# Optimization experiments

Hardware: AMD Instinct MI355X
Metric: run time of the kernel (lower is better)

Reference implementation:

```python
import jax, jax.numpy as jnp
import numpy as np


def setup_inputs() -> dict:
    key = jax.random.key(0)
    k1, k2, k3, k4 = jax.random.split(key, 4)
    B, S, D = 32, 512, 768
    return {
        "image": jax.random.normal(k1, (B, S, D), dtype=jnp.float32),
        "text": jax.random.normal(k2, (B, S, D), dtype=jnp.float32),
        "target": jax.random.normal(k3, (B, S, D), dtype=jnp.float32),
        "padding_mask": jax.random.randint(k4, (B, S), 0, 2, dtype=jnp.int32),
    }


def reference(image, text, target, padding_mask):
    D = image.shape[-1]
    # Drop BOS / CLS position for the text<->target alignment.
    txt = text[:, 1:]                      # [B, S-1, D]
    tgt = target[:, 1:]                    # [B, S-1, D]
    pm = padding_mask[:, 1:]               # [B, S-1]

    # Cosine similarity: normalize then batched matmul.
    txt_n = txt / jnp.linalg.norm(txt, axis=-1, keepdims=True)
    tgt_n = tgt / jnp.linalg.norm(tgt, axis=-1, keepdims=True)
    sim = jnp.einsum('bid,bjd->bij', txt_n, tgt_n)   # [B, S-1, S-1]

    # For each text token, pick the best-matching target patch.
    idx = jnp.argmax(sim, axis=-1)                   # [B, S-1]
    aligned = jnp.take_along_axis(tgt, idx[..., None], axis=1)  # [B, S-1, D]

    # Masked MSE over non-padded tokens (mask==1 means padded in torch code).
    valid = (pm == 0).astype(jnp.float32)            # [B, S-1]
    diff2 = jnp.square(txt.astype(jnp.float32) - aligned.astype(jnp.float32))
    kd_text_loss = jnp.sum(diff2 * valid[..., None]) / (jnp.sum(valid) * D)

    # Plain MSE between image tokens and full target.
    kd_image_loss = jnp.mean(jnp.square(image.astype(jnp.float32) - target.astype(jnp.float32)))

    total_loss = (kd_text_loss + kd_image_loss) / 2
    return total_loss, kd_text_loss, kd_image_loss, idx
```

## Files before the change

kernel.cpp:

```cpp
#include <hip/hip_runtime.h>
#include <math.h>

#define B       32
#define S_FULL  512
#define S       511
#define D       768
#define NROWS   (B * S)

#define TM 128
#define TN 128
#define NCHUNK 4
#define NKT 24
#define EPS_MARGIN 6e-5f
#define SIM_SCALE  512.0f

typedef __attribute__((ext_vector_type(8))) _Float16 f16x8;
typedef __attribute__((ext_vector_type(4))) float f32x4;

__device__ inline void cvt8(const float4& v0, const float4& v1, float s,
                            f16x8& hv, f16x8& lv, float& nacc) {
    float x[8] = {v0.x, v0.y, v0.z, v0.w, v1.x, v1.y, v1.z, v1.w};
    #pragma unroll
    for (int e = 0; e < 8; e += 2) {
        float xa = x[e] * s, xb = x[e + 1] * s;
        nacc = fmaf(xa, xa, nacc);
        nacc = fmaf(xb, xb, nacc);
        auto h = __builtin_amdgcn_cvt_pkrtz(xa, xb);
        auto l = __builtin_amdgcn_cvt_pkrtz(xa - (float)h.x, xb - (float)h.y);
        hv[e] = (_Float16)h.x; hv[e + 1] = (_Float16)h.y;
        lv[e] = (_Float16)l.x; lv[e + 1] = (_Float16)l.y;
    }
}

__global__ __launch_bounds__(256) void prep_kernel(
    const float* __restrict__ image, const float* __restrict__ target,
    float* __restrict__ acc)
{
    int row  = blockIdx.x * 4 + (threadIdx.x >> 6);
    int lane = threadIdx.x & 63;
    const float4* pi4 = (const float4*)(image  + (size_t)row * D);
    const float4* pg4 = (const float4*)(target + (size_t)row * D);
    float si = 0.f;
    #pragma unroll
    for (int q = 0; q < 3; ++q) {
        float4 m = pi4[lane + 64 * q];
        float4 g = pg4[lane + 64 * q];
        float dx = m.x-g.x, dy = m.y-g.y, dz = m.z-g.z, dw = m.w-g.w;
        si += dx*dx + dy*dy + dz*dz + dw*dw;
    }
    #pragma unroll
    for (int m = 32; m > 0; m >>= 1) si += __shfl_xor(si, m);
    if (lane == 0) atomicAdd(&acc[blockIdx.x & 63], si);
}

__global__ __launch_bounds__(256, 2) void simargmax_kernel(
    const float* __restrict__ text, const float* __restrict__ target,
    float* __restrict__ inv_g,
    float* __restrict__ pv, float* __restrict__ ps, int* __restrict__ pj)
{
    __shared__ __align__(16) _Float16 As[2][TM * 64];
    __shared__ __align__(16) _Float16 Bs[2][TM * 64];
    __shared__ float itL[TM], igL[TM];

    const int i0 = blockIdx.x * TM;
    const int jc = blockIdx.y;
    const int j0 = jc * TN;
    const int b  = blockIdx.z;
    const int t  = threadIdx.x;
    const int lane = t & 63;
    const int wy = t >> 6;
    const int quad = lane >> 4, cid = lane & 15;

    const float* Abase = text   + (size_t)b * S_FULL * D + D;
    const float* Bbase = target + (size_t)b * S_FULL * D + D;

    const int r0 = t >> 2;
    const int c0 = t & 3;
    const int kq = c0 * 8;

    const int sw8 = (r0 & 7) * 8;
    const int fw8 = (cid & 7) * 8;
    const int qh  = quad * 8;

    float na[2] = {0.f, 0.f}, nb[2] = {0.f, 0.f};

    f32x4 acc[2][8];
    #pragma unroll
    for (int mt = 0; mt < 2; ++mt)
        #pragma unroll
        for (int nt = 0; nt < 8; ++nt)
            acc[mt][nt] = (f32x4){0.f, 0.f, 0.f, 0.f};

    float4 va[2][2], vb[2][2];
    auto loadk = [&](int kt) {
        const int k0 = kt * 32;
        #pragma unroll
        for (int h = 0; h < 2; ++h) {
            int gi = i0 + r0 + 64 * h;
            if (gi < S) {
                const float4* pa = (const float4*)(Abase + (size_t)gi * D + k0 + kq);
                va[h][0] = pa[0]; va[h][1] = pa[1];
            } else {
                va[h][0] = make_float4(0.f,0.f,0.f,0.f);
                va[h][1] = make_float4(0.f,0.f,0.f,0.f);
            }
            int gj = j0 + r0 + 64 * h;
            if (gj < S) {
                const float4* pb = (const float4*)(Bbase + (size_t)gj * D + k0 + kq);
                vb[h][0] = pb[0]; vb[h][1] = pb[1];
            } else {
                vb[h][0] = make_float4(0.f,0.f,0.f,0.f);
                vb[h][1] = make_float4(0.f,0.f,0.f,0.f);
            }
        }
    };
    auto cvtstore = [&](int p) {
        #pragma unroll
        for (int h = 0; h < 2; ++h) {
            int base = (r0 + 64 * h) * 64;
            f16x8 hv, lv;
            cvt8(va[h][0], va[h][1], SIM_SCALE, hv, lv, na[h]);
            *(f16x8*)&As[p][base + ((c0 * 8)      ^ sw8)] = hv;
            *(f16x8*)&As[p][base + ((32 + c0 * 8) ^ sw8)] = lv;
            cvt8(vb[h][0], vb[h][1], SIM_SCALE, hv, lv, nb[h]);
            *(f16x8*)&Bs[p][base + ((c0 * 8)      ^ sw8)] = hv;
            *(f16x8*)&Bs[p][base + ((32 + c0 * 8) ^ sw8)] = lv;
        }
    };

    loadk(0);
    cvtstore(0);

    for (int kt = 0; kt < NKT; ++kt) {
        const int p = kt & 1;
        if (kt + 1 < NKT) loadk(kt + 1);
        __syncthreads();
        f16x8 ah[2], al[2];
        #pragma unroll
        for (int mt = 0; mt < 2; ++mt) {
            int ad = (wy * 32 + mt * 16 + cid) * 64;
            ah[mt] = *(const f16x8*)&As[p][ad + ( qh       ^ fw8)];
            al[mt] = *(const f16x8*)&As[p][ad + ((32 + qh) ^ fw8)];
        }
        #pragma unroll
        for (int nt = 0; nt < 8; ++nt) {
            int bd = (nt * 16 + cid) * 64;
            f16x8 bh = *(const f16x8*)&Bs[p][bd + ( qh       ^ fw8)];
            f16x8 bl = *(const f16x8*)&Bs[p][bd + ((32 + qh) ^ fw8)];
            #pragma unroll
            for (int mt = 0; mt < 2; ++mt) {
                acc[mt][nt] = __builtin_amdgcn_mfma_f32_16x16x32_f16(ah[mt], bh, acc[mt][nt], 0, 0, 0);
                acc[mt][nt] = __builtin_amdgcn_mfma_f32_16x16x32_f16(ah[mt], bl, acc[mt][nt], 0, 0, 0);
                acc[mt][nt] = __builtin_amdgcn_mfma_f32_16x16x32_f16(al[mt], bh, acc[mt][nt], 0, 0, 0);
            }
        }
        if (kt + 1 < NKT) cvtstore(p ^ 1);
    }

    float* fsA = (float*)&As[0][0];
    float* fsB = fsA + 4 * TM;
    #pragma unroll
    for (int h = 0; h < 2; ++h) {
        fsA[(r0 + 64 * h) * 4 + c0] = na[h];
        fsB[(r0 + 64 * h) * 4 + c0] = nb[h];
    }
    __syncthreads();
    if (t < TM) {
        float s = fsA[t*4] + fsA[t*4+1] + fsA[t*4+2] + fsA[t*4+3];
        itL[t] = (s > 0.f) ? (1.f / sqrtf(s)) : 0.f;
    } else {
        int r = t - TM;
        float s = fsB[r*4] + fsB[r*4+1] + fsB[r*4+2] + fsB[r*4+3];
        float ig = (s > 0.f) ? (1.f / sqrtf(s)) : 0.f;
        igL[r] = ig;
        if (i0 == 0) {
            int gj = j0 + r;
            if (gj < S) inv_g[b * S + gj] = ig;
        }
    }
    __syncthreads();

    float igr[8];
    #pragma unroll
    for (int nt = 0; nt < 8; ++nt) igr[nt] = igL[nt * 16 + cid];
    #pragma unroll
    for (int mt = 0; mt < 2; ++mt) {
        #pragma unroll
        for (int r = 0; r < 4; ++r) {
            float v1 = -INFINITY, v2 = -INFINITY; int j1 = -1;
            #pragma unroll
            for (int nt = 0; nt < 8; ++nt) {
                int col = j0 + nt * 16 + cid;
                float v = acc[mt][nt][r] * igr[nt];
                if (col < S) {
                    if (v > v1) { v2 = v1; v1 = v; j1 = col; }
                    else if (v > v2) v2 = v;
                }
            }
            #pragma unroll
            for (int m = 1; m < 16; m <<= 1) {
                float ov1 = __shfl_xor(v1, m);
                int   oj1 = __shfl_xor(j1, m);
                float ov2 = __shfl_xor(v2, m);
                if (ov1 > v1) { v2 = fmaxf(v1, ov2); v1 = ov1; j1 = oj1; }
                else          { v2 = fmaxf(v2, ov1); }
            }
            if (cid == 0) {
                int lrow = wy * 32 + mt * 16 + quad * 4 + r;
                int gi = i0 + lrow;
                if (gi < S) {
                    float it = itL[lrow];
                    size_t o = ((size_t)(b * S + gi) << 2) + jc;
                    pv[o] = v1 * it; ps[o] = v2 * it; pj[o] = j1;
                }
            }
        }
    }
}

__global__ __launch_bounds__(256) void text_kernel(
    const float* __restrict__ text, const float* __restrict__ target,
    const int* __restrict__ pm,
    const float* __restrict__ pv, const float* __restrict__ ps, const int* __restrict__ pj,
    float* __restrict__ idx_f, float* __restrict__ acc,
    int* __restrict__ list, int* __restrict__ cnt)
{
    int row = blockIdx.x * 4 + (threadIdx.x >> 6);
    if (row >= NROWS) return;
    int lane = threadIdx.x & 63;
    int b = row / S, i = row - b * S;

    float v1 = -INFINITY, v2 = -INFINITY; int j1 = 0;
    #pragma unroll
    for (int c = 0; c < NCHUNK; ++c) {
        size_t o = ((size_t)row << 2) + c;
        float a1 = pv[o], a2 = ps[o]; int aj = pj[o];
        if (a1 > v1) { v2 = fmaxf(v1, a2); v1 = a1; j1 = aj; }
        else         { v2 = fmaxf(v2, a1); }
    }
    if (v1 - v2 < EPS_MARGIN) {
        if (lane == 0) { int p = atomicAdd(cnt, 1); list[p] = row; }
        return;
    }
    if (lane == 0) idx_f[row] = (float)j1;

    if (pm[b * S_FULL + i + 1] != 0) return;
    const float4* pt = (const float4*)(text   + (size_t)(b * S_FULL + i  + 1) * D);
    const float4* pg = (const float4*)(target + (size_t)(b * S_FULL + j1 + 1) * D);
    float s = 0.f;
    #pragma unroll
    for (int q = 0; q < 3; ++q) {
        float4 a = pt[lane + 64 * q];
        float4 g = pg[lane + 64 * q];
        float dx = a.x-g.x, dy = a.y-g.y, dz = a.z-g.z, dw = a.w-g.w;
        s += dx*dx + dy*dy + dz*dz + dw*dw;
    }
    #pragma unroll
    for (int m = 32; m > 0; m >>= 1) s += __shfl_xor(s, m);
    if (lane == 0) {
        atomicAdd(&acc[64  + (blockIdx.x & 63)], s);
        atomicAdd(&acc[128 + (blockIdx.x & 63)], 1.0f);
    }
}

__global__ __launch_bounds__(256) void recheck_kernel(
    const float* __restrict__ text, const float* __restrict__ target,
    const int* __restrict__ pm, const float* __restrict__ inv_g,
    const int* __restrict__ list, const int* __restrict__ cnt,
    float* __restrict__ idx_f, float* __restrict__ acc)
{
    __shared__ float wv[4];
    __shared__ int   wj[4];
    __shared__ int   bjf;
    const int t = threadIdx.x, w = t >> 6, lane = t & 63;
    const int n = *cnt;
    for (int it = blockIdx.x; it < n; it += gridDim.x) {
        int row = list[it];
        int b = row / S, i = row - b * S;
        const float4* tp = (const float4*)(text + (size_t)(b * S_FULL + i + 1) * D);
        float4 tr0 = tp[lane], tr1 = tp[lane + 64], tr2 = tp[lane + 128];
        const float* Gb = target + (size_t)b * S_FULL * D + D;
        const float* ig = inv_g + b * S;

        float bv = -INFINITY; int bj = 0;
        for (int j = w; j < S; j += 8) {
            const float4* g0 = (const float4*)(Gb + (size_t)j * D);
            int j2 = j + 4; bool ok2 = (j2 < S);
            const float4* g1 = (const float4*)(Gb + (size_t)(ok2 ? j2 : j) * D);
            float4 a0 = g0[lane], a1 = g0[lane + 64], a2 = g0[lane + 128];
            float4 c0 = g1[lane], c1 = g1[lane + 64], c2 = g1[lane + 128];
            float s0 = tr0.x*a0.x + tr0.y*a0.y + tr0.z*a0.z + tr0.w*a0.w
                     + tr1.x*a1.x + tr1.y*a1.y + tr1.z*a1.z + tr1.w*a1.w
                     + tr2.x*a2.x + tr2.y*a2.y + tr2.z*a2.z + tr2.w*a2.w;
            float s1 = tr0.x*c0.x + tr0.y*c0.y + tr0.z*c0.z + tr0.w*c0.w
                     + tr1.x*c1.x + tr1.y*c1.y + tr1.z*c1.z + tr1.w*c1.w
                     + tr2.x*c2.x + tr2.y*c2.y + tr2.z*c2.z + tr2.w*c2.w;
            #pragma unroll
            for (int m = 32; m > 0; m >>= 1) {
                s0 += __shfl_xor(s0, m);
                s1 += __shfl_xor(s1, m);
            }
            s0 *= ig[j];
            if (s0 > bv) { bv = s0; bj = j; }
            if (ok2) {
                s1 *= ig[j2];
                if (s1 > bv) { bv = s1; bj = j2; }
            }
        }
        if (lane == 0) { wv[w] = bv; wj[w] = bj; }
        __syncthreads();
        if (t == 0) {
            float fv = wv[0]; int fj = wj[0];
            #pragma unroll
            for (int q = 1; q < 4; ++q)
                if (wv[q] > fv || (wv[q] == fv && wj[q] < fj)) { fv = wv[q]; fj = wj[q]; }
            bjf = fj;
            idx_f[row] = (float)fj;
        }
        __syncthreads();
        if (w == 0 && pm[b * S_FULL + i + 1] == 0) {
            const float4* gp = (const float4*)(Gb + (size_t)bjf * D);
            float4 a0 = gp[lane], a1 = gp[lane + 64], a2 = gp[lane + 128];
            float dx, s = 0.f;
            dx = tr0.x-a0.x; s += dx*dx;  dx = tr0.y-a0.y; s += dx*dx;
            dx = tr0.z-a0.z; s += dx*dx;  dx = tr0.w-a0.w; s += dx*dx;
            dx = tr1.x-a1.x; s += dx*dx;  dx = tr1.y-a1.y; s += dx*dx;
            dx = tr1.z-a1.z; s += dx*dx;  dx = tr1.w-a1.w; s += dx*dx;
            dx = tr2.x-a2.x; s += dx*dx;  dx = tr2.y-a2.y; s += dx*dx;
            dx = tr2.z-a2.z; s += dx*dx;  dx = tr2.w-a2.w; s += dx*dx;
            #pragma unroll
            for (int m = 32; m > 0; m >>= 1) s += __shfl_xor(s, m);
            if (lane == 0) {
                atomicAdd(&acc[64  + (blockIdx.x & 63)], s);
                atomicAdd(&acc[128 + (blockIdx.x & 63)], 1.0f);
            }
        }
        __syncthreads();
    }
}

__global__ void finalize_kernel(const float* __restrict__ acc, float* __restrict__ out)
{
    int lane = threadIdx.x;
    float si = acc[lane], st = acc[64 + lane], sc = acc[128 + lane];
    #pragma unroll
    for (int m = 32; m > 0; m >>= 1) {
        si += __shfl_xor(si, m);
        st += __shfl_xor(st, m);
        sc += __shfl_xor(sc, m);
    }
    if (lane == 0) {
        float img = si / (float)((size_t)B * S_FULL * D);
        float txt = st / (sc * (float)D);
        out[0] = 0.5f * (txt + img);
        out[1] = txt;
        out[2] = img;
    }
}

extern "C" void kernel_launch(void* const* d_in, const int* in_sizes, int n_in,
                              void* d_out, int out_size, void* d_ws, size_t ws_size,
                              hipStream_t stream) {
    const float* image  = (const float*)d_in[0];
    const float* text   = (const float*)d_in[1];
    const float* target = (const float*)d_in[2];
    const int*   pm     = (const int*)d_in[3];
    float* out = (float*)d_out;

    float* ws    = (float*)d_ws;
    float* inv_g = ws + NROWS;
    float* pv    = ws + 2 * NROWS;
    float* ps    = ws + 6 * NROWS;
    int*   pj    = (int*)(ws + 10 * NROWS);
    int*   list  = (int*)(ws + 14 * NROWS);
    int*   cnt   = (int*)(ws + 15 * NROWS);
    float* acc   = ws + 15 * NROWS + 64;

    hipMemsetAsync(ws + 15 * NROWS, 0, 256 * sizeof(float), stream);

    prep_kernel<<<B * S_FULL / 4, 256, 0, stream>>>(image, target, acc);
    simargmax_kernel<<<dim3(4, NCHUNK, B), 256, 0, stream>>>(
        text, target, inv_g, pv, ps, pj);
    text_kernel<<<(NROWS + 3) / 4, 256, 0, stream>>>(
        text, target, pm, pv, ps, pj, out + 3, acc, list, cnt);
    recheck_kernel<<<512, 256, 0, stream>>>(
        text, target, pm, inv_g, list, cnt, out + 3, acc);
    finalize_kernel<<<1, 64, 0, stream>>>(acc, out);
}
```

Before: 374.2 us.

## Replace double-buffered LDS pipeline with single-buffered load-sync-compute loop

Removes the double-buffered shared memory staging in the similarity GEMM. Each k-step now loads global data, syncs, converts and stores to one LDS buffer, syncs again, then runs the MFMAs. This halves the LDS footprint, which may allow more resident blocks, but gives up overlap of global loads with MFMA work and adds an extra barrier per iteration.

```diff
diff --git a/kernel.cpp b/kernel.cpp
--- a/kernel.cpp
+++ b/kernel.cpp
@@ -58,8 +58,8 @@
     float* __restrict__ inv_g,
     float* __restrict__ pv, float* __restrict__ ps, int* __restrict__ pj)
 {
-    __shared__ __align__(16) _Float16 As[2][TM * 64];
-    __shared__ __align__(16) _Float16 Bs[2][TM * 64];
+    __shared__ __align__(16) _Float16 As[TM * 64];
+    __shared__ __align__(16) _Float16 Bs[TM * 64];
     __shared__ float itL[TM], igL[TM];
 
     const int i0 = blockIdx.x * TM;
@@ -91,9 +91,9 @@
         for (int nt = 0; nt < 8; ++nt)
             acc[mt][nt] = (f32x4){0.f, 0.f, 0.f, 0.f};
 
-    float4 va[2][2], vb[2][2];
-    auto loadk = [&](int kt) {
+    for (int kt = 0; kt < NKT; ++kt) {
         const int k0 = kt * 32;
+        float4 va[2][2], vb[2][2];
         #pragma unroll
         for (int h = 0; h < 2; ++h) {
             int gi = i0 + r0 + 64 * h;
@@ -113,40 +113,32 @@
                 vb[h][1] = make_float4(0.f,0.f,0.f,0.f);
             }
         }
-    };
-    auto cvtstore = [&](int p) {
+        __syncthreads();
         #pragma unroll
         for (int h = 0; h < 2; ++h) {
             int base = (r0 + 64 * h) * 64;
             f16x8 hv, lv;
             cvt8(va[h][0], va[h][1], SIM_SCALE, hv, lv, na[h]);
-            *(f16x8*)&As[p][base + ((c0 * 8)      ^ sw8)] = hv;
-            *(f16x8*)&As[p][base + ((32 + c0 * 8) ^ sw8)] = lv;
+            *(f16x8*)&As[base + ((c0 * 8)      ^ sw8)] = hv;
+            *(f16x8*)&As[base + ((32 + c0 * 8) ^ sw8)] = lv;
             cvt8(vb[h][0], vb[h][1], SIM_SCALE, hv, lv, nb[h]);
-            *(f16x8*)&Bs[p][base + ((c0 * 8)      ^ sw8)] = hv;
-            *(f16x8*)&Bs[p][base + ((32 + c0 * 8) ^ sw8)] = lv;
-        }
-    };
-
-    loadk(0);
-    cvtstore(0);
-
-    for (int kt = 0; kt < NKT; ++kt) {
-        const int p = kt & 1;
-        if (kt + 1 < NKT) loadk(kt + 1);
-        __syncthreads();
+            *(f16x8*)&Bs[base + ((c0 * 8)      ^ sw8)] = hv;
+            *(f16x8*)&Bs[base + ((32 + c0 * 8) ^ sw8)] = lv;
+        }
+        __syncthreads();
+
         f16x8 ah[2], al[2];
         #pragma unroll
         for (int mt = 0; mt < 2; ++mt) {
             int ad = (wy * 32 + mt * 16 + cid) * 64;
-            ah[mt] = *(const f16x8*)&As[p][ad + ( qh       ^ fw8)];
-            al[mt] = *(const f16x8*)&As[p][ad + ((32 + qh) ^ fw8)];
+            ah[mt] = *(const f16x8*)&As[ad + ( qh       ^ fw8)];
+            al[mt] = *(const f16x8*)&As[ad + ((32 + qh) ^ fw8)];
         }
         #pragma unroll
         for (int nt = 0; nt < 8; ++nt) {
             int bd = (nt * 16 + cid) * 64;
-            f16x8 bh = *(const f16x8*)&Bs[p][bd + ( qh       ^ fw8)];
-            f16x8 bl = *(const f16x8*)&Bs[p][bd + ((32 + qh) ^ fw8)];
+            f16x8 bh = *(const f16x8*)&Bs[bd + ( qh       ^ fw8)];
+            f16x8 bl = *(const f16x8*)&Bs[bd + ((32 + qh) ^ fw8)];
             #pragma unroll
             for (int mt = 0; mt < 2; ++mt) {
                 acc[mt][nt] = __builtin_amdgcn_mfma_f32_16x16x32_f16(ah[mt], bh, acc[mt][nt], 0, 0, 0);
@@ -154,10 +146,10 @@
                 acc[mt][nt] = __builtin_amdgcn_mfma_f32_16x16x32_f16(al[mt], bh, acc[mt][nt], 0, 0, 0);
             }
         }
-        if (kt + 1 < NKT) cvtstore(p ^ 1);
-    }
-
-    float* fsA = (float*)&As[0][0];
+    }
+
+    __syncthreads();
+    float* fsA = (float*)&As[0];
     float* fsB = fsA + 4 * TM;
     #pragma unroll
     for (int h = 0; h < 2; ++h) {
```

New measurement: 377.8 us. No clear change (+1.0%).
